# Kernel optimization log

Hardware: AMD Instinct MI355X
Metric: run time of the kernel (lower is better)

## Reference

```python
import jax, jax.numpy as jnp
import numpy as np

N = 4096   # n_roi
E = 131072 # edges (avg degree 32)
B = 64     # batch of subjects/windows sharing one connectome
K = 4      # Chebyshev order


def _cheb_params(key, cin, cout):
    kw, kb = jax.random.split(key)
    w = jax.random.normal(kw, (K, cin, cout), dtype=jnp.float32) / np.sqrt(K * cin)
    b = jax.random.normal(kb, (cout,), dtype=jnp.float32) * 0.01
    return w, b


def _lin_params(key, cin, cout):
    kw, kb = jax.random.split(key)
    w = jax.random.normal(kw, (cin, cout), dtype=jnp.float32) / np.sqrt(cin)
    b = jax.random.normal(kb, (cout,), dtype=jnp.float32) * 0.01
    return w, b


def setup_inputs() -> dict:
    key = jax.random.key(0)
    ks = jax.random.split(key, 12)
    x = jax.random.normal(ks[0], (B, N, 1), dtype=jnp.float32)
    src = jax.random.randint(ks[1], (E,), 0, N, dtype=jnp.int32)
    dst = jax.random.randint(ks[2], (E,), 0, N, dtype=jnp.int32)
    edge_weight = jax.random.uniform(ks[3], (E,), dtype=jnp.float32)
    w1, b1 = _cheb_params(ks[4], 1, 32)
    w2, b2 = _cheb_params(ks[5], 32, 32)
    w3, b3 = _cheb_params(ks[6], 32, 32)
    w4, b4 = _cheb_params(ks[7], 32, 32)
    w5, b5 = _cheb_params(ks[8], 32, 4)
    fw1, fb1 = _lin_params(ks[9], N * 4, 128)
    fw2, fb2 = _lin_params(ks[10], 128, 128)
    fw3, fb3 = _lin_params(ks[11], 128, 9)
    return dict(x=x, src=src, dst=dst, edge_weight=edge_weight,
                w1=w1, b1=b1, w2=w2, b2=b2, w3=w3, b3=b3,
                w4=w4, b4=b4, w5=w5, b5=b5,
                fw1=fw1, fb1=fb1, fw2=fw2, fb2=fb2, fw3=fw3, fb3=fb3)


def _norm_weights(src, dst, edge_weight):
    # PyG ChebConv default: sym normalization, lambda_max=2 ->
    # L_hat = -D^{-1/2} A D^{-1/2}, diagonal 2/lambda_max - 1 = 0 (self-loop skipped)
    deg = jax.ops.segment_sum(edge_weight, src, num_segments=N)
    dinv = jnp.where(deg > 0, jax.lax.rsqrt(jnp.maximum(deg, 1e-30)), 0.0)
    return -dinv[src] * edge_weight * dinv[dst]


def _propagate(z, src, dst, nw):
    # z: [B, N, C] -> L_hat @ z  via gather-multiply-scatter over edges
    msg = nw[None, :, None] * z[:, src, :]          # [B, E, C]
    msg = jnp.swapaxes(msg, 0, 1)                    # [E, B, C]
    agg = jax.ops.segment_sum(msg, dst, num_segments=N)  # [N, B, C]
    return jnp.swapaxes(agg, 0, 1)                   # [B, N, C]


def _cheb_conv(x, src, dst, nw, w, b):
    # x: [B,N,Cin], w: [K,Cin,Cout]
    tx0 = x
    out = jnp.einsum('bni,io->bno', tx0, w[0])
    tx1 = _propagate(tx0, src, dst, nw)
    out = out + jnp.einsum('bni,io->bno', tx1, w[1])
    for k in range(2, K):
        tx2 = 2.0 * _propagate(tx1, src, dst, nw) - tx0
        out = out + jnp.einsum('bni,io->bno', tx2, w[k])
        tx0, tx1 = tx1, tx2
    return out + b


def reference(x, src, dst, edge_weight, w1, b1, w2, b2, w3, b3, w4, b4, w5, b5,
              fw1, fb1, fw2, fb2, fw3, fb3):
    nw = _norm_weights(src, dst, edge_weight)
    h = jax.nn.relu(_cheb_conv(x, src, dst, nw, w1, b1))
    h = jax.nn.relu(_cheb_conv(h, src, dst, nw, w2, b2))
    h = jax.nn.relu(_cheb_conv(h, src, dst, nw, w3, b3))
    h = jax.nn.relu(_cheb_conv(h, src, dst, nw, w4, b4))
    h = jax.nn.relu(_cheb_conv(h, src, dst, nw, w5, b5))  # [B, N, 4]
    h = h.reshape(B, N * 4)
    # original has dropout (identity at eval) and NO relu between fc layers
    h = h @ fw1 + fb1
    h = h @ fw2 + fb2
    return h @ fw3 + fb3  # [B, 9]
```

## Files before the change

kernel.cpp:

```cpp
#include <hip/hip_runtime.h>
#include <cstdint>

#define NN 4096
#define EE 131072
#define BB 64
#define EPAD (EE + 8 * NN)

typedef float f4 __attribute__((ext_vector_type(4)));
typedef short bf16x8 __attribute__((ext_vector_type(8)));
typedef unsigned short ushort_t;
typedef unsigned int uint_t;

__device__ __forceinline__ void up8(uint4 u, f4& lo, f4& hi) {
    lo.x = __uint_as_float(u.x << 16);
    lo.y = __uint_as_float(u.x & 0xffff0000u);
    lo.z = __uint_as_float(u.y << 16);
    lo.w = __uint_as_float(u.y & 0xffff0000u);
    hi.x = __uint_as_float(u.z << 16);
    hi.y = __uint_as_float(u.z & 0xffff0000u);
    hi.z = __uint_as_float(u.w << 16);
    hi.w = __uint_as_float(u.w & 0xffff0000u);
}
__device__ __forceinline__ uint_t bfpk(float a, float b) {
    uint_t xa = __float_as_uint(a); xa = (xa + 0x7fffu + ((xa >> 16) & 1u)) >> 16;
    uint_t xb = __float_as_uint(b); xb = (xb + 0x7fffu + ((xb >> 16) & 1u));
    return (xa & 0xffffu) | (xb & 0xffff0000u);
}
__device__ __forceinline__ ushort_t bf1(float a) {
    uint_t x = __float_as_uint(a);
    return (ushort_t)((x + 0x7fffu + ((x >> 16) & 1u)) >> 16);
}

__global__ void k_deg_hist(const int* __restrict__ src, const int* __restrict__ dst,
                           const float* __restrict__ ew, float* __restrict__ deg,
                           int* __restrict__ cnt) {
    int e = blockIdx.x * blockDim.x + threadIdx.x;
    if (e >= EE) return;
    atomicAdd(&deg[src[e]], ew[e]);
    atomicAdd(&cnt[dst[e]], 1);
}

__global__ __launch_bounds__(1024) void k_scan(const int* __restrict__ cnt,
                                               int* __restrict__ rowptr,
                                               int* __restrict__ cursor) {
    __shared__ int s[1024];
    int tid = threadIdx.x;
    int p0 = (cnt[tid * 4 + 0] + 7) & ~7;
    int p1 = (cnt[tid * 4 + 1] + 7) & ~7;
    int p2 = (cnt[tid * 4 + 2] + 7) & ~7;
    int p3 = (cnt[tid * 4 + 3] + 7) & ~7;
    int sum = p0 + p1 + p2 + p3;
    s[tid] = sum;
    __syncthreads();
    for (int off = 1; off < 1024; off <<= 1) {
        int t = (tid >= off) ? s[tid - off] : 0;
        __syncthreads();
        s[tid] += t;
        __syncthreads();
    }
    int excl = s[tid] - sum;
    rowptr[tid * 4 + 0] = excl; cursor[tid * 4 + 0] = excl; excl += p0;
    rowptr[tid * 4 + 1] = excl; cursor[tid * 4 + 1] = excl; excl += p1;
    rowptr[tid * 4 + 2] = excl; cursor[tid * 4 + 2] = excl; excl += p2;
    rowptr[tid * 4 + 3] = excl; cursor[tid * 4 + 3] = excl; excl += p3;
    if (tid == 1023) rowptr[4096] = excl;
}

__global__ void k_fill(const int* __restrict__ src, const int* __restrict__ dst,
                       const float* __restrict__ ew, const float* __restrict__ deg,
                       int* __restrict__ cursor, int2* __restrict__ cv) {
    int e = blockIdx.x * blockDim.x + threadIdx.x;
    if (e >= EE) return;
    int s = src[e], d = dst[e];
    int pos = atomicAdd(&cursor[d], 1);
    float ds = deg[s], dd = deg[d];
    float is = ds > 0.f ? rsqrtf(fmaxf(ds, 1e-30f)) : 0.f;
    float id = dd > 0.f ? rsqrtf(fmaxf(dd, 1e-30f)) : 0.f;
    float v = -(is * ew[e] * id);
    cv[pos] = make_int2(s, __float_as_int(v));
}

__global__ __launch_bounds__(256) void k_transpose_x(const float* __restrict__ x,
                                                     float* __restrict__ X0) {
    __shared__ float s[64 * 65];
    int n0 = blockIdx.x * 64;
    for (int idx = threadIdx.x; idx < 4096; idx += 256) {
        int b = idx >> 6, nl = idx & 63;
        s[nl * 65 + b] = x[(size_t)b * NN + n0 + nl];
    }
    __syncthreads();
    for (int idx = threadIdx.x; idx < 4096; idx += 256) {
        int nl = idx >> 6, b = idx & 63;
        X0[(size_t)(n0 + nl) * 64 + b] = s[nl * 65 + b];
    }
}

__global__ __launch_bounds__(64) void k_spmm_narrow(const int* __restrict__ rowptr,
                                                    const int2* __restrict__ cv,
                                                    const float* __restrict__ Zin,
                                                    const float* __restrict__ Tprev,
                                                    float* __restrict__ Tout,
                                                    float alpha, int useprev) {
    int n = blockIdx.x;
    int lane = threadIdx.x;
    int start = rowptr[n], end = rowptr[n + 1];
    float acc = 0.f;
    for (int e = start; e < end; e += 8) {
        const int4* q = reinterpret_cast<const int4*>(cv + e);
        int4 a = q[0], b = q[1], c = q[2], d = q[3];
        float z0 = Zin[((size_t)a.x << 6) + lane];
        float z1 = Zin[((size_t)a.z << 6) + lane];
        float z2 = Zin[((size_t)b.x << 6) + lane];
        float z3 = Zin[((size_t)b.z << 6) + lane];
        float z4 = Zin[((size_t)c.x << 6) + lane];
        float z5 = Zin[((size_t)c.z << 6) + lane];
        float z6 = Zin[((size_t)d.x << 6) + lane];
        float z7 = Zin[((size_t)d.z << 6) + lane];
        acc += __int_as_float(a.y) * z0 + __int_as_float(a.w) * z1
             + __int_as_float(b.y) * z2 + __int_as_float(b.w) * z3
             + __int_as_float(c.y) * z4 + __int_as_float(c.w) * z5
             + __int_as_float(d.y) * z6 + __int_as_float(d.w) * z7;
    }
    size_t o = ((size_t)n << 6) + lane;
    float r = alpha * acc;
    if (useprev) r -= Tprev[o];
    Tout[o] = r;
}

__global__ __launch_bounds__(256) void k_expand1(const float* __restrict__ T0,
                                                 const float* __restrict__ T1,
                                                 const float* __restrict__ T2,
                                                 const float* __restrict__ T3,
                                                 const float* __restrict__ w1,
                                                 const float* __restrict__ b1,
                                                 ushort_t* __restrict__ H) {
    __shared__ float sT[4][64];
    __shared__ float sW[128];
    __shared__ float sB[32];
    int n = blockIdx.x, tid = threadIdx.x;
    {
        int k = tid >> 6, b = tid & 63;
        const float* Tk = (k == 0) ? T0 : (k == 1) ? T1 : (k == 2) ? T2 : T3;
        sT[k][b] = Tk[(size_t)n * 64 + b];
    }
    if (tid < 128) sW[tid] = w1[tid];
    if (tid < 32) sB[tid] = b1[tid];
    __syncthreads();
    int col0 = tid * 8;
    int b = tid >> 2;
    int co0 = col0 & 31;
    float t0 = sT[0][b], t1 = sT[1][b], t2 = sT[2][b], t3 = sT[3][b];
    float r[8];
#pragma unroll
    for (int j = 0; j < 8; ++j) {
        int co = co0 + j;
        float v = t0 * sW[co] + t1 * sW[32 + co] + t2 * sW[64 + co] + t3 * sW[96 + co] + sB[co];
        r[j] = v > 0.f ? v : 0.f;
    }
    uint4 st;
    st.x = bfpk(r[0], r[1]); st.y = bfpk(r[2], r[3]);
    st.z = bfpk(r[4], r[5]); st.w = bfpk(r[6], r[7]);
    *reinterpret_cast<uint4*>(H + (size_t)n * 2048 + col0) = st;
}

__global__ __launch_bounds__(256) void k_spmm_pure(const int* __restrict__ rowptr,
                                                   const int2* __restrict__ cv,
                                                   const ushort_t* __restrict__ Zg,
                                                   const ushort_t* __restrict__ Pown,
                                                   ushort_t* __restrict__ Tout) {
    int chunk = blockIdx.x & 3;
    int rowblk = blockIdx.x >> 2;
    int wave = threadIdx.x >> 6;
    int lane = threadIdx.x & 63;
    int n = rowblk * 4 + wave;
    int col0 = chunk * 512 + lane * 8;

    int start = rowptr[n], end = rowptr[n + 1];
    f4 aL0 = {0,0,0,0}, aH0 = {0,0,0,0}, aL1 = {0,0,0,0}, aH1 = {0,0,0,0};
    for (int e = start; e < end; e += 8) {
        const int4* q = reinterpret_cast<const int4*>(cv + e);
        int4 a = q[0], b = q[1], c = q[2], d = q[3];
        uint4 u0 = *reinterpret_cast<const uint4*>(Zg + (((size_t)a.x) << 11) + col0);
        uint4 u1 = *reinterpret_cast<const uint4*>(Zg + (((size_t)a.z) << 11) + col0);
        uint4 u2 = *reinterpret_cast<const uint4*>(Zg + (((size_t)b.x) << 11) + col0);
        uint4 u3 = *reinterpret_cast<const uint4*>(Zg + (((size_t)b.z) << 11) + col0);
        uint4 u4 = *reinterpret_cast<const uint4*>(Zg + (((size_t)c.x) << 11) + col0);
        uint4 u5 = *reinterpret_cast<const uint4*>(Zg + (((size_t)c.z) << 11) + col0);
        uint4 u6 = *reinterpret_cast<const uint4*>(Zg + (((size_t)d.x) << 11) + col0);
        uint4 u7 = *reinterpret_cast<const uint4*>(Zg + (((size_t)d.z) << 11) + col0);
        f4 lo, hi;
        up8(u0, lo, hi); aL0 += __int_as_float(a.y) * lo; aH0 += __int_as_float(a.y) * hi;
        up8(u1, lo, hi); aL1 += __int_as_float(a.w) * lo; aH1 += __int_as_float(a.w) * hi;
        up8(u2, lo, hi); aL0 += __int_as_float(b.y) * lo; aH0 += __int_as_float(b.y) * hi;
        up8(u3, lo, hi); aL1 += __int_as_float(b.w) * lo; aH1 += __int_as_float(b.w) * hi;
        up8(u4, lo, hi); aL0 += __int_as_float(c.y) * lo; aH0 += __int_as_float(c.y) * hi;
        up8(u5, lo, hi); aL1 += __int_as_float(c.w) * lo; aH1 += __int_as_float(c.w) * hi;
        up8(u6, lo, hi); aL0 += __int_as_float(d.y) * lo; aH0 += __int_as_float(d.y) * hi;
        up8(u7, lo, hi); aL1 += __int_as_float(d.w) * lo; aH1 += __int_as_float(d.w) * hi;
    }
    size_t o = (((size_t)n) << 11) + col0;
    f4 tL = aL0 + aL1, tH = aH0 + aH1;
    if (Pown) {
        uint4 pu = *reinterpret_cast<const uint4*>(Pown + o);
        f4 pL, pH;
        up8(pu, pL, pH);
        tL = 2.f * tL - pL;
        tH = 2.f * tH - pH;
    }
    uint4 st;
    st.x = bfpk(tL.x, tL.y); st.y = bfpk(tL.z, tL.w);
    st.z = bfpk(tH.x, tH.y); st.w = bfpk(tH.z, tH.w);
    *reinterpret_cast<uint4*>(Tout + o) = st;
}

template <int COUT, bool OUTBF>
__global__ __launch_bounds__(256, 5) void k_cheb_out(
    const int* __restrict__ rowptr, const int2* __restrict__ cv,
    const ushort_t* __restrict__ T2g,
    const ushort_t* __restrict__ T1,
    const ushort_t* __restrict__ H,
    const float* __restrict__ W,
    const float* __restrict__ bias,
    void* __restrict__ OUTv)
{
    __shared__ uint_t sPu[4][4][320];
    __shared__ uint_t sWb[(COUT == 32) ? 2560 : 1];
    __shared__ float  sWf[(COUT == 4) ? 512 : 1];

    int chunk = blockIdx.x & 3;
    int rowblk = blockIdx.x >> 2;
    int wave = threadIdx.x >> 6;
    int lane = threadIdx.x & 63;
    int n = rowblk * 4 + wave;
    int col0 = chunk * 512 + lane * 8;
    int tid = threadIdx.x;

    if constexpr (COUT == 32) {
        for (int idx = tid; idx < 2048; idx += 256) {
            int p = idx >> 9, rem = idx & 511;
            int co = rem >> 4, u = rem & 15;
            sWb[p * 640 + co * 20 + u] =
                bfpk(W[p * 1024 + (2 * u) * 32 + co], W[p * 1024 + (2 * u + 1) * 32 + co]);
        }
    } else {
        for (int idx = tid; idx < 4 * 32 * COUT; idx += 256) sWf[idx] = W[idx];
    }

    int start = rowptr[n], end = rowptr[n + 1];
    f4 aL0 = {0,0,0,0}, aH0 = {0,0,0,0}, aL1 = {0,0,0,0}, aH1 = {0,0,0,0};
    for (int e = start; e < end; e += 8) {
        const int4* q = reinterpret_cast<const int4*>(cv + e);
        int4 a = q[0], b = q[1], c = q[2], d = q[3];
        uint4 u0 = *reinterpret_cast<const uint4*>(T2g + (((size_t)a.x) << 11) + col0);
        uint4 u1 = *reinterpret_cast<const uint4*>(T2g + (((size_t)a.z) << 11) + col0);
        uint4 u2 = *reinterpret_cast<const uint4*>(T2g + (((size_t)b.x) << 11) + col0);
        uint4 u3 = *reinterpret_cast<const uint4*>(T2g + (((size_t)b.z) << 11) + col0);
        uint4 u4 = *reinterpret_cast<const uint4*>(T2g + (((size_t)c.x) << 11) + col0);
        uint4 u5 = *reinterpret_cast<const uint4*>(T2g + (((size_t)c.z) << 11) + col0);
        uint4 u6 = *reinterpret_cast<const uint4*>(T2g + (((size_t)d.x) << 11) + col0);
        uint4 u7 = *reinterpret_cast<const uint4*>(T2g + (((size_t)d.z) << 11) + col0);
        f4 lo, hi;
        up8(u0, lo, hi); aL0 += __int_as_float(a.y) * lo; aH0 += __int_as_float(a.y) * hi;
        up8(u1, lo, hi); aL1 += __int_as_float(a.w) * lo; aH1 += __int_as_float(a.w) * hi;
        up8(u2, lo, hi); aL0 += __int_as_float(b.y) * lo; aH0 += __int_as_float(b.y) * hi;
        up8(u3, lo, hi); aL1 += __int_as_float(b.w) * lo; aH1 += __int_as_float(b.w) * hi;
        up8(u4, lo, hi); aL0 += __int_as_float(c.y) * lo; aH0 += __int_as_float(c.y) * hi;
        up8(u5, lo, hi); aL1 += __int_as_float(c.w) * lo; aH1 += __int_as_float(c.w) * hi;
        up8(u6, lo, hi); aL0 += __int_as_float(d.y) * lo; aH0 += __int_as_float(d.y) * hi;
        up8(u7, lo, hi); aL1 += __int_as_float(d.w) * lo; aH1 += __int_as_float(d.w) * hi;
    }
    size_t o = (((size_t)n) << 11) + col0;

    int g = lane >> 2, qd = lane & 3;
    int si = g * 20 + qd * 4;
    {
        uint4 pu = *reinterpret_cast<const uint4*>(T1 + o);
        f4 pL, pH;
        up8(pu, pL, pH);
        f4 tL = 2.f * (aL0 + aL1) - pL;
        f4 tH = 2.f * (aH0 + aH1) - pH;
        uint4 st;
        st.x = bfpk(tL.x, tL.y); st.y = bfpk(tL.z, tL.w);
        st.z = bfpk(tH.x, tH.y); st.w = bfpk(tH.z, tH.w);
        *reinterpret_cast<uint4*>(&sPu[wave][3][si]) = st;
        *reinterpret_cast<uint4*>(&sPu[wave][1][si]) = pu;
    }
    *reinterpret_cast<uint4*>(&sPu[wave][2][si]) =
        *reinterpret_cast<const uint4*>(T2g + o);
    *reinterpret_cast<uint4*>(&sPu[wave][0][si]) =
        *reinterpret_cast<const uint4*>(H + o);
    __syncthreads();

    if constexpr (COUT == 32) {
        int mr = lane & 15;
        int qk = lane >> 4;
        f4 accA = {0,0,0,0}, accB = {0,0,0,0};
#pragma unroll
        for (int kk = 0; kk < 4; ++kk) {
            bf16x8 af = *reinterpret_cast<const bf16x8*>(&sPu[wave][kk][mr * 20 + qk * 4]);
            bf16x8 b0 = *reinterpret_cast<const bf16x8*>(&sWb[kk * 640 + mr * 20 + qk * 4]);
            bf16x8 b1 = *reinterpret_cast<const bf16x8*>(&sWb[kk * 640 + (16 + mr) * 20 + qk * 4]);
            accA = __builtin_amdgcn_mfma_f32_16x16x32_bf16(af, b0, accA, 0, 0, 0);
            accB = __builtin_amdgcn_mfma_f32_16x16x32_bf16(af, b1, accB, 0, 0, 0);
        }
        int co = lane & 15;
        float bA = bias[co], bB = bias[co + 16];
        ushort_t* OB = (ushort_t*)OUTv;
        size_t obase = (((size_t)n) << 11) + chunk * 512;
#pragma unroll
        for (int r = 0; r < 4; ++r) {
            int gb = (lane >> 4) * 4 + r;
            float vA = accA[r] + bA;
            float vB = accB[r] + bB;
            vA = vA > 0.f ? vA : 0.f;
            vB = vB > 0.f ? vB : 0.f;
            OB[obase + gb * 32 + co]      = bf1(vA);
            OB[obase + gb * 32 + co + 16] = bf1(vB);
        }
    } else {
        int co = lane & 3;
        float o0 = 0.f;
#pragma unroll
        for (int u = 0; u < 16; ++u) {
#pragma unroll
            for (int p = 0; p < 4; ++p) {
                uint_t au = sPu[wave][p][g * 20 + u];
                float alo = __uint_as_float(au << 16);
                float ahi = __uint_as_float(au & 0xffff0000u);
                o0 += alo * sWf[p * 128 + (2 * u) * 4 + co]
                    + ahi * sWf[p * 128 + (2 * u + 1) * 4 + co];
            }
        }
        float r = o0 + bias[co];
        r = r > 0.f ? r : 0.f;
        ((float*)OUTv)[n * 256 + chunk * 64 + lane] = r;
    }
}

__global__ __launch_bounds__(256) void k_fc1(const float* __restrict__ H5,
                                             const float* __restrict__ fw1,
                                             float* __restrict__ fc1out) {
    __shared__ float hT[128 * 65];
    __shared__ float wS[32 * 128];
    int tid = threadIdx.x;
    int n0 = blockIdx.x * 32;
    for (int idx = tid; idx < 8192; idx += 256) {
        int n_l = idx >> 8;
        int rem = idx & 255;
        int b = rem >> 2, c = rem & 3;
        int kk = n_l * 4 + c;
        hT[kk * 65 + b] = H5[(size_t)(n0 + n_l) * 256 + rem];
    }
    float acc[8][4];
#pragma unroll
    for (int i = 0; i < 8; ++i)
#pragma unroll
        for (int j = 0; j < 4; ++j) acc[i][j] = 0.f;
    int bq = tid >> 5;
    int jq = tid & 31;
    for (int kb = 0; kb < 128; kb += 32) {
        __syncthreads();
        for (int idx = tid; idx < 4096; idx += 256) {
            int kl = idx >> 7, j = idx & 127;
            wS[idx] = fw1[(size_t)(n0 * 4 + kb + kl) * 128 + j];
        }
        __syncthreads();
        for (int kl = 0; kl < 32; ++kl) {
            int kk = kb + kl;
            float4 w = *reinterpret_cast<const float4*>(&wS[kl * 128 + jq * 4]);
#pragma unroll
            for (int bi = 0; bi < 8; ++bi) {
                float h = hT[kk * 65 + bq * 8 + bi];
                acc[bi][0] += h * w.x;
                acc[bi][1] += h * w.y;
                acc[bi][2] += h * w.z;
                acc[bi][3] += h * w.w;
            }
        }
    }
#pragma unroll
    for (int bi = 0; bi < 8; ++bi)
#pragma unroll
        for (int ji = 0; ji < 4; ++ji)
            atomicAdd(&fc1out[(bq * 8 + bi) * 128 + jq * 4 + ji], acc[bi][ji]);
}

__global__ __launch_bounds__(128) void k_fc23(const float* __restrict__ fc1out,
                                              const float* __restrict__ fb1,
                                              const float* __restrict__ fw2,
                                              const float* __restrict__ fb2,
                                              const float* __restrict__ fw3,
                                              const float* __restrict__ fb3,
                                              float* __restrict__ out) {
    int b = blockIdx.x;
    int j = threadIdx.x;
    __shared__ float r[128];
    __shared__ float s1[128];
    r[j] = fc1out[b * 128 + j] + fb1[j];
    __syncthreads();
    float acc = fb2[j];
    for (int i = 0; i < 128; ++i) acc += r[i] * fw2[i * 128 + j];
    s1[j] = acc;
    __syncthreads();
    if (j < 9) {
        float a2 = fb3[j];
        for (int i = 0; i < 128; ++i) a2 += s1[i] * fw3[i * 9 + j];
        out[b * 9 + j] = a2;
    }
}

extern "C" void kernel_launch(void* const* d_in, const int* in_sizes, int n_in,
                              void* d_out, int out_size, void* d_ws, size_t ws_size,
                              hipStream_t stream) {
    const float* x   = (const float*)d_in[0];
    const int*   src = (const int*)d_in[1];
    const int*   dst = (const int*)d_in[2];
    const float* ew  = (const float*)d_in[3];
    const float* w1  = (const float*)d_in[4];
    const float* b1  = (const float*)d_in[5];
    const float* w2  = (const float*)d_in[6];
    const float* b2  = (const float*)d_in[7];
    const float* w3  = (const float*)d_in[8];
    const float* b3  = (const float*)d_in[9];
    const float* w4  = (const float*)d_in[10];
    const float* b4  = (const float*)d_in[11];
    const float* w5  = (const float*)d_in[12];
    const float* b5  = (const float*)d_in[13];
    const float* fw1 = (const float*)d_in[14];
    const float* fb1 = (const float*)d_in[15];
    const float* fw2 = (const float*)d_in[16];
    const float* fb2 = (const float*)d_in[17];
    const float* fw3 = (const float*)d_in[18];
    const float* fb3 = (const float*)d_in[19];
    float* out = (float*)d_out;

    char* p = (char*)d_ws;
    const size_t XBYTES = (size_t)NN * 2048 * 2;
    ushort_t* X0 = (ushort_t*)(p + 0 * XBYTES);
    ushort_t* X1 = (ushort_t*)(p + 1 * XBYTES);
    ushort_t* X2 = (ushort_t*)(p + 2 * XBYTES);
    ushort_t* X3 = (ushort_t*)(p + 3 * XBYTES);
    size_t off = 4 * XBYTES;
    float* H5     = (float*)(p + off); off += (size_t)NN * 256 * 4;
    float* deg    = (float*)(p + off); off += (size_t)NN * 4;
    int*   cnt    = (int*)(p + off);   off += (size_t)NN * 4;
    int*   cursor = (int*)(p + off);   off += (size_t)NN * 4;
    int*   rowptr = (int*)(p + off);   off += (size_t)(NN + 4) * 4;
    int2*  cv     = (int2*)(p + off);  off += (size_t)EPAD * 8;
    float* fc1o   = (float*)(p + off); off += (size_t)BB * 128 * 4;
    float* xn0    = (float*)(p + off); off += (size_t)NN * 64 * 4;
    float* tn1    = (float*)(p + off); off += (size_t)NN * 64 * 4;
    float* tn2    = (float*)(p + off); off += (size_t)NN * 64 * 4;
    float* tn3    = (float*)(p + off); off += (size_t)NN * 64 * 4;
    if (off > ws_size) return;

    hipMemsetAsync(deg, 0, NN * 4, stream);
    hipMemsetAsync(cnt, 0, NN * 4, stream);
    hipMemsetAsync(cv, 0, (size_t)EPAD * 8, stream);
    hipMemsetAsync(fc1o, 0, BB * 128 * 4, stream);

    k_deg_hist<<<EE / 256, 256, 0, stream>>>(src, dst, ew, deg, cnt);
    k_scan<<<1, 1024, 0, stream>>>(cnt, rowptr, cursor);
    k_fill<<<EE / 256, 256, 0, stream>>>(src, dst, ew, deg, cursor, cv);
    k_transpose_x<<<NN / 64, 256, 0, stream>>>(x, xn0);

    k_spmm_narrow<<<NN, 64, 0, stream>>>(rowptr, cv, xn0, nullptr, tn1, 1.f, 0);
    k_spmm_narrow<<<NN, 64, 0, stream>>>(rowptr, cv, tn1, xn0, tn2, 2.f, 1);
    k_spmm_narrow<<<NN, 64, 0, stream>>>(rowptr, cv, tn2, tn1, tn3, 2.f, 1);
    k_expand1<<<NN, 256, 0, stream>>>(xn0, tn1, tn2, tn3, w1, b1, X3);

    const int GRID4 = (NN / 4) * 4;
    auto run32 = [&](const ushort_t* H, ushort_t* T1, ushort_t* T2, ushort_t* OUT,
                     const float* W, const float* B) {
        k_spmm_pure<<<GRID4, 256, 0, stream>>>(rowptr, cv, H, nullptr, T1);
        k_spmm_pure<<<GRID4, 256, 0, stream>>>(rowptr, cv, T1, H, T2);
        k_cheb_out<32, true><<<GRID4, 256, 0, stream>>>(rowptr, cv, T2, T1, H, W, B, OUT);
    };
    run32(X3, X0, X1, X2, w2, b2);
    run32(X2, X3, X0, X1, w3, b3);
    run32(X1, X2, X3, X0, w4, b4);

    k_spmm_pure<<<GRID4, 256, 0, stream>>>(rowptr, cv, X0, nullptr, X1);
    k_spmm_pure<<<GRID4, 256, 0, stream>>>(rowptr, cv, X1, X0, X2);
    k_cheb_out<4, false><<<GRID4, 256, 0, stream>>>(rowptr, cv, X2, X1, X0, w5, b5, H5);

    k_fc1<<<128, 256, 0, stream>>>(H5, fw1, fc1o);
    k_fc23<<<BB, 128, 0, stream>>>(fc1o, fb1, fw2, fb2, fw3, fb3, out);
}
```

Before: 640.5 us.

## Prepack Chebyshev weights once and feed MFMA directly from registers

A new kernel packs the bf16 weights for layers 2-5 into a global buffer once, so each Chebyshev output block no longer converts weights itself. Each lane's column mapping is changed so its gathered features already form the MFMA A-fragment. This removes the shared-memory staging and the __syncthreads. The final 4-channel layer now also uses MFMA with zero-padded weights instead of a scalar dot-product loop. The cost is an extra launch and per-lane global weight loads, which should mostly hit cache. The gather access pattern also changes, which may affect coalescing.

```diff
diff --git a/kernel.cpp b/kernel.cpp
--- a/kernel.cpp
+++ b/kernel.cpp
@@ -78,6 +78,26 @@
     float id = dd > 0.f ? rsqrtf(fmaxf(dd, 1e-30f)) : 0.f;
     float v = -(is * ew[e] * id);
     cv[pos] = make_int2(s, __float_as_int(v));
+}
+
+__global__ __launch_bounds__(256) void k_packw(const float* __restrict__ w2,
+                                               const float* __restrict__ w3,
+                                               const float* __restrict__ w4,
+                                               const float* __restrict__ w5,
+                                               uint_t* __restrict__ Wb) {
+    int idx = blockIdx.x * 256 + threadIdx.x;
+    int L = idx >> 11, rem = idx & 2047;
+    int kk = rem >> 9, r2 = rem & 511, co = r2 >> 4, u = r2 & 15;
+    float lo, hi;
+    if (L < 3) {
+        const float* W = (L == 0) ? w2 : (L == 1) ? w3 : w4;
+        lo = W[kk * 1024 + (2 * u) * 32 + co];
+        hi = W[kk * 1024 + (2 * u + 1) * 32 + co];
+    } else {
+        lo = (co < 4) ? w5[kk * 128 + (2 * u) * 4 + co] : 0.f;
+        hi = (co < 4) ? w5[kk * 128 + (2 * u + 1) * 4 + co] : 0.f;
+    }
+    Wb[idx] = bfpk(lo, hi);
 }
 
 __global__ __launch_bounds__(256) void k_transpose_x(const float* __restrict__ x,
@@ -213,38 +233,23 @@
     *reinterpret_cast<uint4*>(Tout + o) = st;
 }
 
-template <int COUT, bool OUTBF>
-__global__ __launch_bounds__(256, 5) void k_cheb_out(
+template <int COUT>
+__global__ __launch_bounds__(256) void k_cheb_mfma(
     const int* __restrict__ rowptr, const int2* __restrict__ cv,
     const ushort_t* __restrict__ T2g,
     const ushort_t* __restrict__ T1,
     const ushort_t* __restrict__ H,
-    const float* __restrict__ W,
+    const uint_t* __restrict__ Wb,
     const float* __restrict__ bias,
     void* __restrict__ OUTv)
 {
-    __shared__ uint_t sPu[4][4][320];
-    __shared__ uint_t sWb[(COUT == 32) ? 2560 : 1];
-    __shared__ float  sWf[(COUT == 4) ? 512 : 1];
-
     int chunk = blockIdx.x & 3;
     int rowblk = blockIdx.x >> 2;
     int wave = threadIdx.x >> 6;
     int lane = threadIdx.x & 63;
     int n = rowblk * 4 + wave;
-    int col0 = chunk * 512 + lane * 8;
-    int tid = threadIdx.x;
-
-    if constexpr (COUT == 32) {
-        for (int idx = tid; idx < 2048; idx += 256) {
-            int p = idx >> 9, rem = idx & 511;
-            int co = rem >> 4, u = rem & 15;
-            sWb[p * 640 + co * 20 + u] =
-                bfpk(W[p * 1024 + (2 * u) * 32 + co], W[p * 1024 + (2 * u + 1) * 32 + co]);
-        }
-    } else {
-        for (int idx = tid; idx < 4 * 32 * COUT; idx += 256) sWf[idx] = W[idx];
-    }
+    int b16 = lane & 15, qk = lane >> 4;
+    int col0 = chunk * 512 + b16 * 32 + qk * 8;
 
     int start = rowptr[n], end = rowptr[n + 1];
     f4 aL0 = {0,0,0,0}, aH0 = {0,0,0,0}, aL1 = {0,0,0,0}, aH1 = {0,0,0,0};
@@ -271,45 +276,43 @@
     }
     size_t o = (((size_t)n) << 11) + col0;
 
-    int g = lane >> 2, qd = lane & 3;
-    int si = g * 20 + qd * 4;
+    uint4 a1 = *reinterpret_cast<const uint4*>(T1 + o);
+    uint4 a3;
     {
-        uint4 pu = *reinterpret_cast<const uint4*>(T1 + o);
         f4 pL, pH;
-        up8(pu, pL, pH);
+        up8(a1, pL, pH);
         f4 tL = 2.f * (aL0 + aL1) - pL;
         f4 tH = 2.f * (aH0 + aH1) - pH;
-        uint4 st;
-        st.x = bfpk(tL.x, tL.y); st.y = bfpk(tL.z, tL.w);
-        st.z = bfpk(tH.x, tH.y); st.w = bfpk(tH.z, tH.w);
-        *reinterpret_cast<uint4*>(&sPu[wave][3][si]) = st;
-        *reinterpret_cast<uint4*>(&sPu[wave][1][si]) = pu;
-    }
-    *reinterpret_cast<uint4*>(&sPu[wave][2][si]) =
-        *reinterpret_cast<const uint4*>(T2g + o);
-    *reinterpret_cast<uint4*>(&sPu[wave][0][si]) =
-        *reinterpret_cast<const uint4*>(H + o);
-    __syncthreads();
-
+        a3.x = bfpk(tL.x, tL.y); a3.y = bfpk(tL.z, tL.w);
+        a3.z = bfpk(tH.x, tH.y); a3.w = bfpk(tH.z, tH.w);
+    }
+    uint4 a2 = *reinterpret_cast<const uint4*>(T2g + o);
+    uint4 a0 = *reinterpret_cast<const uint4*>(H + o);
+
+    const uint_t* wb = Wb + b16 * 16 + qk * 4;
+    f4 accA = {0,0,0,0}, accB = {0,0,0,0};
+#pragma unroll
+    for (int kk = 0; kk < 4; ++kk) {
+        uint4 af4 = (kk == 0) ? a0 : (kk == 1) ? a1 : (kk == 2) ? a2 : a3;
+        bf16x8 af = *reinterpret_cast<bf16x8*>(&af4);
+        uint4 w0 = *reinterpret_cast<const uint4*>(wb + kk * 512);
+        bf16x8 bf0 = *reinterpret_cast<bf16x8*>(&w0);
+        accA = __builtin_amdgcn_mfma_f32_16x16x32_bf16(af, bf0, accA, 0, 0, 0);
+        if constexpr (COUT == 32) {
+            uint4 w1 = *reinterpret_cast<const uint4*>(wb + kk * 512 + 256);
+            bf16x8 bf1_ = *reinterpret_cast<bf16x8*>(&w1);
+            accB = __builtin_amdgcn_mfma_f32_16x16x32_bf16(af, bf1_, accB, 0, 0, 0);
+        }
+    }
+
+    int co = lane & 15;
     if constexpr (COUT == 32) {
-        int mr = lane & 15;
-        int qk = lane >> 4;
-        f4 accA = {0,0,0,0}, accB = {0,0,0,0};
-#pragma unroll
-        for (int kk = 0; kk < 4; ++kk) {
-            bf16x8 af = *reinterpret_cast<const bf16x8*>(&sPu[wave][kk][mr * 20 + qk * 4]);
-            bf16x8 b0 = *reinterpret_cast<const bf16x8*>(&sWb[kk * 640 + mr * 20 + qk * 4]);
-            bf16x8 b1 = *reinterpret_cast<const bf16x8*>(&sWb[kk * 640 + (16 + mr) * 20 + qk * 4]);
-            accA = __builtin_amdgcn_mfma_f32_16x16x32_bf16(af, b0, accA, 0, 0, 0);
-            accB = __builtin_amdgcn_mfma_f32_16x16x32_bf16(af, b1, accB, 0, 0, 0);
-        }
-        int co = lane & 15;
         float bA = bias[co], bB = bias[co + 16];
         ushort_t* OB = (ushort_t*)OUTv;
         size_t obase = (((size_t)n) << 11) + chunk * 512;
 #pragma unroll
         for (int r = 0; r < 4; ++r) {
-            int gb = (lane >> 4) * 4 + r;
+            int gb = qk * 4 + r;
             float vA = accA[r] + bA;
             float vB = accB[r] + bB;
             vA = vA > 0.f ? vA : 0.f;
@@ -318,22 +321,18 @@
             OB[obase + gb * 32 + co + 16] = bf1(vB);
         }
     } else {
-        int co = lane & 3;
-        float o0 = 0.f;
-#pragma unroll
-        for (int u = 0; u < 16; ++u) {
-#pragma unroll
-            for (int p = 0; p < 4; ++p) {
-                uint_t au = sPu[wave][p][g * 20 + u];
-                float alo = __uint_as_float(au << 16);
-                float ahi = __uint_as_float(au & 0xffff0000u);
-                o0 += alo * sWf[p * 128 + (2 * u) * 4 + co]
-                    + ahi * sWf[p * 128 + (2 * u + 1) * 4 + co];
+        if (co < 4) {
+            float bA = bias[co];
+            float* OF = (float*)OUTv;
+            size_t obase = (size_t)n * 256 + chunk * 64;
+#pragma unroll
+            for (int r = 0; r < 4; ++r) {
+                int gb = qk * 4 + r;
+                float vA = accA[r] + bA;
+                vA = vA > 0.f ? vA : 0.f;
+                OF[obase + gb * 4 + co] = vA;
             }
         }
-        float r = o0 + bias[co];
-        r = r > 0.f ? r : 0.f;
-        ((float*)OUTv)[n * 256 + chunk * 64 + lane] = r;
     }
 }
 
@@ -452,6 +451,7 @@
     float* tn1    = (float*)(p + off); off += (size_t)NN * 64 * 4;
     float* tn2    = (float*)(p + off); off += (size_t)NN * 64 * 4;
     float* tn3    = (float*)(p + off); off += (size_t)NN * 64 * 4;
+    uint_t* Wb    = (uint_t*)(p + off); off += (size_t)4 * 2048 * 4;
     if (off > ws_size) return;
 
     hipMemsetAsync(deg, 0, NN * 4, stream);
@@ -462,6 +462,7 @@
     k_deg_hist<<<EE / 256, 256, 0, stream>>>(src, dst, ew, deg, cnt);
     k_scan<<<1, 1024, 0, stream>>>(cnt, rowptr, cursor);
     k_fill<<<EE / 256, 256, 0, stream>>>(src, dst, ew, deg, cursor, cv);
+    k_packw<<<32, 256, 0, stream>>>(w2, w3, w4, w5, Wb);
     k_transpose_x<<<NN / 64, 256, 0, stream>>>(x, xn0);
 
     k_spmm_narrow<<<NN, 64, 0, stream>>>(rowptr, cv, xn0, nullptr, tn1, 1.f, 0);
@@ -471,18 +472,18 @@
 
     const int GRID4 = (NN / 4) * 4;
     auto run32 = [&](const ushort_t* H, ushort_t* T1, ushort_t* T2, ushort_t* OUT,
-                     const float* W, const float* B) {
+                     const uint_t* WbL, const float* B) {
         k_spmm_pure<<<GRID4, 256, 0, stream>>>(rowptr, cv, H, nullptr, T1);
         k_spmm_pure<<<GRID4, 256, 0, stream>>>(rowptr, cv, T1, H, T2);
-        k_cheb_out<32, true><<<GRID4, 256, 0, stream>>>(rowptr, cv, T2, T1, H, W, B, OUT);
+        k_cheb_mfma<32><<<GRID4, 256, 0, stream>>>(rowptr, cv, T2, T1, H, WbL, B, OUT);
     };
-    run32(X3, X0, X1, X2, w2, b2);
-    run32(X2, X3, X0, X1, w3, b3);
-    run32(X1, X2, X3, X0, w4, b4);
+    run32(X3, X0, X1, X2, Wb + 0 * 2048, b2);
+    run32(X2, X3, X0, X1, Wb + 1 * 2048, b3);
+    run32(X1, X2, X3, X0, Wb + 2 * 2048, b4);
 
     k_spmm_pure<<<GRID4, 256, 0, stream>>>(rowptr, cv, X0, nullptr, X1);
     k_spmm_pure<<<GRID4, 256, 0, stream>>>(rowptr, cv, X1, X0, X2);
-    k_cheb_out<4, false><<<GRID4, 256, 0, stream>>>(rowptr, cv, X2, X1, X0, w5, b5, H5);
+    k_cheb_mfma<4><<<GRID4, 256, 0, stream>>>(rowptr, cv, X2, X1, X0, Wb + 3 * 2048, b5, H5);
 
     k_fc1<<<128, 256, 0, stream>>>(H5, fw1, fc1o);
     k_fc23<<<BB, 128, 0, stream>>>(fc1o, fb1, fw2, fb2, fw3, fb3, out);
```

New measurement: 628.9 us. About the same (-1.8%).
